# Performance work log

Hardware: AMD Instinct MI355X
Metric: run time of the kernel (lower is better)

The kernel has to match this reference:

```python
import jax, jax.numpy as jnp
from jax import lax
import numpy as np

EPS = 1e-12  # matches torch F.normalize eps


def _dtw_similarity(s1, s2):
    # s1: [L1, D], s2: [L2, D]
    L1, L2 = s1.shape[0], s2.shape[0]
    s1n = s1 / jnp.maximum(jnp.linalg.norm(s1, axis=1, keepdims=True), EPS)
    s2n = s2 / jnp.maximum(jnp.linalg.norm(s2, axis=1, keepdims=True), EPS)
    dist = 1.0 - s1n @ s2n.T  # [L1, L2] cosine distance

    # DTW DP. Row 0 is a cumsum; each subsequent row has a left-to-right
    # sequential dependency handled by an inner scan.
    row0 = jnp.cumsum(dist[0])

    def row_step(prev_row, d_row):
        # prev_row: dtw[i-1, :], d_row: dist[i, :]
        first = prev_row[0] + d_row[0]  # dtw[i, 0]
        # min(prev[j], prev[j-1]) for j >= 1 (vectorized part of the min)
        p = jnp.minimum(prev_row[1:], prev_row[:-1])

        def col_step(c, inp):
            dj, pj = inp
            new = dj + jnp.minimum(pj, c)  # c = dtw[i, j-1]
            return new, new

        _, rest = lax.scan(col_step, first, (d_row[1:], p))
        new_row = jnp.concatenate([first[None], rest])
        return new_row, None

    last_row, _ = lax.scan(row_step, row0, dist[1:])
    dtw_distance = last_row[-1]
    normalized = dtw_distance / (L1 + L2)
    return 1.0 / (1.0 + normalized)


def setup_inputs() -> dict:
    key = jax.random.key(0)
    k1, k2 = jax.random.split(key)
    seq1 = jax.random.normal(k1, (16, 1024, 768), dtype=jnp.float32)
    seq2 = jax.random.normal(k2, (16, 1024, 768), dtype=jnp.float32)
    return {"seq1": seq1, "seq2": seq2}


def reference(seq1, seq2):
    # seq1: [B, L1, D], seq2: [B, L2, D] -> [B]
    return jax.vmap(_dtw_similarity)(seq1, seq2)
```

## Files before the change

### kernel.cpp

```cpp
#include <hip/hip_runtime.h>
#include <hip/hip_bf16.h>

typedef __attribute__((ext_vector_type(4))) float f32x4;
typedef __attribute__((ext_vector_type(8))) short bf16x8;

#define DINF 1e30f

__device__ __forceinline__ unsigned short f2bf(float f) {
    unsigned int u = __builtin_bit_cast(unsigned int, f);
    u += 0x7FFFu + ((u >> 16) & 1u);
    return (unsigned short)(u >> 16);
}

__global__ __launch_bounds__(256) void zero_holes_kernel(float4* __restrict__ skew) {
    const int idx = blockIdx.x;
    const int bt  = idx / 127;
    const int pr  = idx % 127;
    const int h   = pr * 2 + (threadIdx.x >> 7);
    const int row = h < 126 ? h : 1024 + (h - 126);
    const int c   = threadIdx.x & 127;
    skew[((size_t)bt * 1152 + row) * 128 + c] = (float4){0.f, 0.f, 0.f, 0.f};
}

__global__ __launch_bounds__(256) void norm_bf16_kernel(
    const float* __restrict__ s1, const float* __restrict__ s2,
    __hip_bfloat16* __restrict__ o1, __hip_bfloat16* __restrict__ o2) {
    const int gb = blockIdx.x;
    const float* in;
    __hip_bfloat16* out;
    int rowbase;
    if (gb < 4096) { in = s1; out = o1; rowbase = gb * 4; }
    else           { in = s2; out = o2; rowbase = (gb - 4096) * 4; }
    const int wv = threadIdx.x >> 6;
    const int l  = threadIdx.x & 63;
    const int row = rowbase + wv;

    const float* rp = in + (size_t)row * 768 + l * 4;
    float4 x0 = *(const float4*)(rp);
    float4 x1 = *(const float4*)(rp + 256);
    float4 x2 = *(const float4*)(rp + 512);

    float s = x0.x*x0.x + x0.y*x0.y + x0.z*x0.z + x0.w*x0.w
            + x1.x*x1.x + x1.y*x1.y + x1.z*x1.z + x1.w*x1.w
            + x2.x*x2.x + x2.y*x2.y + x2.z*x2.z + x2.w*x2.w;
#pragma unroll
    for (int off = 32; off > 0; off >>= 1) s += __shfl_xor(s, off, 64);

    const float inv = 1.0f / fmaxf(sqrtf(s), 1e-12f);

    __hip_bfloat16* op = out + (size_t)row * 768 + l * 4;
    ushort4 o;
    o.x = f2bf(x0.x*inv); o.y = f2bf(x0.y*inv); o.z = f2bf(x0.z*inv); o.w = f2bf(x0.w*inv);
    *(ushort4*)(op) = o;
    o.x = f2bf(x1.x*inv); o.y = f2bf(x1.y*inv); o.z = f2bf(x1.z*inv); o.w = f2bf(x1.w*inv);
    *(ushort4*)(op + 256) = o;
    o.x = f2bf(x2.x*inv); o.y = f2bf(x2.y*inv); o.z = f2bf(x2.z*inv); o.w = f2bf(x2.w*inv);
    *(ushort4*)(op + 512) = o;
}

#define GLOAD_LDS16(g, l)                                                      \
    __builtin_amdgcn_global_load_lds(                                          \
        (const __attribute__((address_space(1))) void*)(g),                    \
        (__attribute__((address_space(3))) void*)(l), 16, 0, 0)

__global__ __launch_bounds__(256) void gemm_dist_kernel(
    const __hip_bfloat16* __restrict__ A, const __hip_bfloat16* __restrict__ B,
    __hip_bfloat16* __restrict__ skew) {
    __shared__ __hip_bfloat16 lA[128 * 64];
    __shared__ __hip_bfloat16 lB[128 * 64];

    const int blk  = (blockIdx.x & 7) * 128 + (blockIdx.x >> 3);
    const int b    = blk >> 6;
    const int tile = blk & 63;
    const int tm = tile >> 3, tn = tile & 7;
    const int tid  = threadIdx.x;
    const int lane = tid & 63, w = tid >> 6;
    const int lr = lane & 15, lg = lane >> 4;
    const int wm = w >> 1, wn = w & 1;

    const __hip_bfloat16* Ab = A + (size_t)b * (1024 * 768) + (size_t)(tm * 128) * 768;
    const __hip_bfloat16* Bb = B + (size_t)b * (1024 * 768) + (size_t)(tn * 128) * 768;

    const int srow = tid >> 3;
    const int scol = (tid & 7) * 8;

    char* lAb = (char*)lA;
    char* lBb = (char*)lB;

    f32x4 acc[4][4];
#pragma unroll
    for (int m = 0; m < 4; ++m)
#pragma unroll
        for (int n = 0; n < 4; ++n) acc[m][n] = (f32x4){0.f, 0.f, 0.f, 0.f};

    for (int k0 = 0; k0 < 768; k0 += 64) {
#pragma unroll
        for (int q = 0; q < 4; ++q) {
            GLOAD_LDS16(Ab + (size_t)(q * 32 + srow) * 768 + k0 + scol,
                        lAb + q * 4096 + w * 1024);
            GLOAD_LDS16(Bb + (size_t)(q * 32 + srow) * 768 + k0 + scol,
                        lBb + q * 4096 + w * 1024);
        }
        __syncthreads();

#pragma unroll
        for (int ks = 0; ks < 64; ks += 32) {
            bf16x8 af[4], bfr[4];
#pragma unroll
            for (int m = 0; m < 4; ++m)
                af[m] = *(const bf16x8*)&lA[(wm * 64 + m * 16 + lr) * 64 + ks + lg * 8];
#pragma unroll
            for (int n = 0; n < 4; ++n)
                bfr[n] = *(const bf16x8*)&lB[(wn * 64 + n * 16 + lr) * 64 + ks + lg * 8];
#pragma unroll
            for (int m = 0; m < 4; ++m)
#pragma unroll
                for (int n = 0; n < 4; ++n)
                    acc[m][n] = __builtin_amdgcn_mfma_f32_16x16x32_bf16(af[m], bfr[n], acc[m][n], 0, 0, 0);
        }
        __syncthreads();
    }

    unsigned short* S = (unsigned short*)skew + (size_t)b * (1152 * 1024);
#pragma unroll
    for (int m = 0; m < 4; ++m)
#pragma unroll
        for (int n = 0; n < 4; ++n) {
            const int cb = tn * 128 + wn * 64 + n * 16;
            const int soff = 2 * (cb >> 4);
#pragma unroll
            for (int r = 0; r < 4; ++r) {
                const int row = tm * 128 + wm * 64 + m * 16 + lg * 4 + r;
                S[(size_t)(row + soff) * 1024 + cb + lr] = f2bf(1.0f - acc[m][n][r]);
            }
        }
}


#define VWAIT(n) asm volatile("s_waitcnt vmcnt(" #n ")" ::: "memory")

#define GLDMA16(g, l)                                                          \
    __builtin_amdgcn_global_load_lds(                                          \
        (const __attribute__((address_space(1))) void*)(g),                    \
        (__attribute__((address_space(3))) void*)(l), 16, 0, 0)

#define LOADR(BK, SL, RW) do {                                                 \
    const char* g_ = Sb + ((size_t)(RW) << 11);                                \
    GLDMA16(g_,      &ring[BK][SL][0][0]);                                     \
    GLDMA16(g_ + 16, &ring[BK][SL][1][0]);                                     \
} while (0)

#define ISSUE8(BK, BASE) do {                                                  \
    LOADR(BK, 0, (BASE));     LOADR(BK, 1, (BASE) + 1);                        \
    LOADR(BK, 2, (BASE) + 2); LOADR(BK, 3, (BASE) + 3);                        \
    LOADR(BK, 4, (BASE) + 4); LOADR(BK, 5, (BASE) + 5);                        \
    LOADR(BK, 6, (BASE) + 6); LOADR(BK, 7, (BASE) + 7);                        \
} while (0)

#define DSRD(BK, SL, N) do {                                                   \
    N##_0 = ring[BK][SL][0][t]; N##_1 = ring[BK][SL][1][t];                    \
} while (0)

#define STEPBODY(P, E0EXPR) do {                                               \
    unsigned u0_ = __builtin_bit_cast(unsigned, P##_0.x);                      \
    unsigned u1_ = __builtin_bit_cast(unsigned, P##_0.y);                      \
    unsigned u2_ = __builtin_bit_cast(unsigned, P##_0.z);                      \
    unsigned u3_ = __builtin_bit_cast(unsigned, P##_0.w);                      \
    unsigned u4_ = __builtin_bit_cast(unsigned, P##_1.x);                      \
    unsigned u5_ = __builtin_bit_cast(unsigned, P##_1.y);                      \
    unsigned u6_ = __builtin_bit_cast(unsigned, P##_1.z);                      \
    unsigned u7_ = __builtin_bit_cast(unsigned, P##_1.w);                      \
    float d0_  = __builtin_bit_cast(float, u0_ << 16);                         \
    float d1_  = __builtin_bit_cast(float, u0_ & 0xffff0000u);                 \
    float d2_  = __builtin_bit_cast(float, u1_ << 16);                         \
    float d3_  = __builtin_bit_cast(float, u1_ & 0xffff0000u);                 \
    float d4_  = __builtin_bit_cast(float, u2_ << 16);                         \
    float d5_  = __builtin_bit_cast(float, u2_ & 0xffff0000u);                 \
    float d6_  = __builtin_bit_cast(float, u3_ << 16);                         \
    float d7_  = __builtin_bit_cast(float, u3_ & 0xffff0000u);                 \
    float d8_  = __builtin_bit_cast(float, u4_ << 16);                         \
    float d9_  = __builtin_bit_cast(float, u4_ & 0xffff0000u);                 \
    float d10_ = __builtin_bit_cast(float, u5_ << 16);                         \
    float d11_ = __builtin_bit_cast(float, u5_ & 0xffff0000u);                 \
    float d12_ = __builtin_bit_cast(float, u6_ << 16);                         \
    float d13_ = __builtin_bit_cast(float, u6_ & 0xffff0000u);                 \
    float d14_ = __builtin_bit_cast(float, u7_ << 16);                         \
    float d15_ = __builtin_bit_cast(float, u7_ & 0xffff0000u);                 \
    float e0_ = (E0EXPR);                                                      \
    float c0_  = d0_  + e0_;                                                   \
    float c1_  = d1_  + fminf(fminf(p1,  p0),  c0_);                           \
    float c2_  = d2_  + fminf(fminf(p2,  p1),  c1_);                           \
    float c3_  = d3_  + fminf(fminf(p3,  p2),  c2_);                           \
    float c4_  = d4_  + fminf(fminf(p4,  p3),  c3_);                           \
    float c5_  = d5_  + fminf(fminf(p5,  p4),  c4_);                           \
    float c6_  = d6_  + fminf(fminf(p6,  p5),  c5_);                           \
    float c7_  = d7_  + fminf(fminf(p7,  p6),  c6_);                           \
    float c8_  = d8_  + fminf(fminf(p8,  p7),  c7_);                           \
    float c9_  = d9_  + fminf(fminf(p9,  p8),  c8_);                           \
    float c10_ = d10_ + fminf(fminf(p10, p9),  c9_);                           \
    float c11_ = d11_ + fminf(fminf(p11, p10), c10_);                          \
    float c12_ = d12_ + fminf(fminf(p12, p11), c11_);                          \
    float c13_ = d13_ + fminf(fminf(p13, p12), c12_);                          \
    float c14_ = d14_ + fminf(fminf(p14, p13), c13_);                          \
    float c15_ = d15_ + fminf(fminf(p15, p14), c14_);                          \
    p0=c0_; p1=c1_; p2=c2_; p3=c3_; p4=c4_; p5=c5_; p6=c6_; p7=c7_;            \
    p8=c8_; p9=c9_; p10=c10_; p11=c11_; p12=c12_; p13=c13_; p14=c14_; p15=c15_;\
    a3 = a2; a2 = a1;                                                          \
    a1 = __shfl_up(c15_, 1, 64);                                               \
    a1 = lane0 ? DINF : a1;                                                    \
} while (0)

#define STEPB(P)       STEPBODY(P, fminf(fminf(p0, a3), a2))
#define STEPB_FIRST(P) STEPBODY(P, lane0 ? 0.0f : fminf(fminf(p0, a3), a2))

__global__ __launch_bounds__(64, 1) void dtw_dp_kernel(
    const __hip_bfloat16* __restrict__ skew, float* __restrict__ out) {
    __shared__ float4 ring[3][8][2][64];

    const int b = blockIdx.x;
    const int t = threadIdx.x;
    const bool lane0 = (t == 0);
    const char* Sb = (const char*)(skew + (size_t)b * (1152 * 1024)) + (t << 5);

    float p0 = DINF, p1 = DINF, p2 = DINF, p3 = DINF,
          p4 = DINF, p5 = DINF, p6 = DINF, p7 = DINF,
          p8 = DINF, p9 = DINF, p10 = DINF, p11 = DINF,
          p12 = DINF, p13 = DINF, p14 = DINF, p15 = DINF;
    float a1 = DINF, a2 = DINF, a3 = DINF;

    float4 X_0, X_1;
    float4 Y_0, Y_1;

    ISSUE8(0, 0);
    ISSUE8(1, 8);
    VWAIT(16);
    DSRD(0, 0, X); DSRD(0, 1, Y);

    ISSUE8(2, 16);
    STEPB_FIRST(X); DSRD(0, 2, X);
    STEPB(Y);       DSRD(0, 3, Y);
    STEPB(X);       DSRD(0, 4, X);
    STEPB(Y);       DSRD(0, 5, Y);
    STEPB(X);       DSRD(0, 6, X);
    STEPB(Y);       DSRD(0, 7, Y);
    VWAIT(16);
    STEPB(X);       DSRD(1, 0, X);
    STEPB(Y);       DSRD(1, 1, Y);

    int rb = 1, nb = 2, ib = 0, base = 24;
#pragma unroll 1
    for (int j = 1; j < 142; ++j) {
        ISSUE8(ib, base);
        STEPB(X); DSRD(rb, 2, X);
        STEPB(Y); DSRD(rb, 3, Y);
        STEPB(X); DSRD(rb, 4, X);
        STEPB(Y); DSRD(rb, 5, Y);
        STEPB(X); DSRD(rb, 6, X);
        STEPB(Y); DSRD(rb, 7, Y);
        VWAIT(16);
        STEPB(X); DSRD(nb, 0, X);
        STEPB(Y); DSRD(nb, 1, Y);
        const int orb = rb;
        rb = nb; nb = ib; ib = orb;
        base += 8;
    }

    STEPB(X); DSRD(1, 2, X);
    STEPB(Y); DSRD(1, 3, Y);
    STEPB(X); DSRD(1, 4, X);
    STEPB(Y); DSRD(1, 5, Y);
    STEPB(X); DSRD(1, 6, X);
    STEPB(Y); DSRD(1, 7, Y);
    VWAIT(0);
    STEPB(X); DSRD(2, 0, X);
    STEPB(Y); DSRD(2, 1, Y);

    STEPB(X); DSRD(2, 2, X);
    STEPB(Y); DSRD(2, 3, Y);
    STEPB(X); DSRD(2, 4, X);
    STEPB(Y); DSRD(2, 5, Y);
    STEPB(X);
    STEPB(Y);

    if (t == 63) out[b] = 1.0f / (1.0f + p15 * (1.0f / 2048.0f));
}

extern "C" void kernel_launch(void* const* d_in, const int* in_sizes, int n_in,
                              void* d_out, int out_size, void* d_ws, size_t ws_size,
                              hipStream_t stream) {
    const float* s1 = (const float*)d_in[0];
    const float* s2 = (const float*)d_in[1];
    float* out = (float*)d_out;

    char* ws = (char*)d_ws;
    __hip_bfloat16* Abf  = (__hip_bfloat16*)(ws);
    __hip_bfloat16* Bbf  = (__hip_bfloat16*)(ws + 25165824);
    __hip_bfloat16* skew = (__hip_bfloat16*)(ws + 50331648);

    zero_holes_kernel<<<16 * 127, 256, 0, stream>>>((float4*)skew);
    norm_bf16_kernel<<<8192, 256, 0, stream>>>(s1, s2, Abf, Bbf);
    gemm_dist_kernel<<<16 * 64, 256, 0, stream>>>(Abf, Bbf, skew);
    dtw_dp_kernel<<<16, 64, 0, stream>>>(skew, out);
}
```

Baseline: 248.2 us.

## Split DTW wavefront across two waves with LDS boundary exchange

The DP kernel now uses two 64-lane waves per batch. Each lane owns 8 columns instead of 16, and the two waves pass boundary values through a shared-memory ring guarded by barriers. The skewed distance layout is widened to 1296 rows so the second wave's staggered start fits, and the hole-zeroing kernel is replaced by a full hipMemsetAsync of the larger buffer. This halves the serial per-step dependency chain per lane, at the cost of a barrier every 8 steps, more wavefront steps, and a larger memset.

```diff
diff --git a/kernel.cpp b/kernel.cpp
--- a/kernel.cpp
+++ b/kernel.cpp
@@ -10,16 +10,6 @@
     unsigned int u = __builtin_bit_cast(unsigned int, f);
     u += 0x7FFFu + ((u >> 16) & 1u);
     return (unsigned short)(u >> 16);
-}
-
-__global__ __launch_bounds__(256) void zero_holes_kernel(float4* __restrict__ skew) {
-    const int idx = blockIdx.x;
-    const int bt  = idx / 127;
-    const int pr  = idx % 127;
-    const int h   = pr * 2 + (threadIdx.x >> 7);
-    const int row = h < 126 ? h : 1024 + (h - 126);
-    const int c   = threadIdx.x & 127;
-    skew[((size_t)bt * 1152 + row) * 128 + c] = (float4){0.f, 0.f, 0.f, 0.f};
 }
 
 __global__ __launch_bounds__(256) void norm_bf16_kernel(
@@ -121,13 +111,14 @@
         __syncthreads();
     }
 
-    unsigned short* S = (unsigned short*)skew + (size_t)b * (1152 * 1024);
+    unsigned short* S = (unsigned short*)skew + (size_t)b * (1296 * 1024);
 #pragma unroll
     for (int m = 0; m < 4; ++m)
 #pragma unroll
         for (int n = 0; n < 4; ++n) {
             const int cb = tn * 128 + wn * 64 + n * 16;
-            const int soff = 2 * (cb >> 4);
+            const int sbase = ((cb >> 3) << 1) + ((cb >> 9) << 4);
+            const int soff  = sbase + ((lr >> 3) << 1);
 #pragma unroll
             for (int r = 0; r < 4; ++r) {
                 const int row = tm * 128 + wm * 64 + m * 16 + lg * 4 + r;
@@ -138,17 +129,14 @@
 
 
 #define VWAIT(n) asm volatile("s_waitcnt vmcnt(" #n ")" ::: "memory")
+#define SBAR()   asm volatile("s_waitcnt lgkmcnt(0)\n\ts_barrier" ::: "memory")
 
 #define GLDMA16(g, l)                                                          \
     __builtin_amdgcn_global_load_lds(                                          \
         (const __attribute__((address_space(1))) void*)(g),                    \
         (__attribute__((address_space(3))) void*)(l), 16, 0, 0)
 
-#define LOADR(BK, SL, RW) do {                                                 \
-    const char* g_ = Sb + ((size_t)(RW) << 11);                                \
-    GLDMA16(g_,      &ring[BK][SL][0][0]);                                     \
-    GLDMA16(g_ + 16, &ring[BK][SL][1][0]);                                     \
-} while (0)
+#define LOADR(BK, SL, RW) GLDMA16(Sb + ((size_t)(RW) << 11), &ring[w][BK][SL][0])
 
 #define ISSUE8(BK, BASE) do {                                                  \
     LOADR(BK, 0, (BASE));     LOADR(BK, 1, (BASE) + 1);                        \
@@ -157,83 +145,78 @@
     LOADR(BK, 6, (BASE) + 6); LOADR(BK, 7, (BASE) + 7);                        \
 } while (0)
 
-#define DSRD(BK, SL, N) do {                                                   \
-    N##_0 = ring[BK][SL][0][t]; N##_1 = ring[BK][SL][1][t];                    \
+#define DSRD(BK, SL, N) do { N = ring[w][BK][SL][t]; } while (0)
+
+#define STEPCORE(P, E0EXPR) do {                                               \
+    float bf_ = bndp[ro];                         \
+    unsigned u0_ = __builtin_bit_cast(unsigned, P.x);                          \
+    unsigned u1_ = __builtin_bit_cast(unsigned, P.y);                          \
+    unsigned u2_ = __builtin_bit_cast(unsigned, P.z);                          \
+    unsigned u3_ = __builtin_bit_cast(unsigned, P.w);                          \
+    float d0_ = __builtin_bit_cast(float, u0_ << 16);                          \
+    float d1_ = __builtin_bit_cast(float, u0_ & 0xffff0000u);                  \
+    float d2_ = __builtin_bit_cast(float, u1_ << 16);                          \
+    float d3_ = __builtin_bit_cast(float, u1_ & 0xffff0000u);                  \
+    float d4_ = __builtin_bit_cast(float, u2_ << 16);                          \
+    float d5_ = __builtin_bit_cast(float, u2_ & 0xffff0000u);                  \
+    float d6_ = __builtin_bit_cast(float, u3_ << 16);                          \
+    float d7_ = __builtin_bit_cast(float, u3_ & 0xffff0000u);                  \
+    float e0_ = (E0EXPR);                                                      \
+    float c0_ = d0_ + e0_;                                                     \
+    float c1_ = d1_ + fminf(fminf(p1, p0), c0_);                               \
+    float c2_ = d2_ + fminf(fminf(p2, p1), c1_);                               \
+    float c3_ = d3_ + fminf(fminf(p3, p2), c2_);                               \
+    float c4_ = d4_ + fminf(fminf(p4, p3), c3_);                               \
+    float c5_ = d5_ + fminf(fminf(p5, p4), c4_);                               \
+    float c6_ = d6_ + fminf(fminf(p6, p5), c5_);                               \
+    float c7_ = d7_ + fminf(fminf(p7, p6), c6_);                               \
+    bndp[wo] = c7_;                 \
+    p0=c0_; p1=c1_; p2=c2_; p3=c3_; p4=c4_; p5=c5_; p6=c6_; p7=c7_;            \
+    a3 = a2; a2 = a1;                                                          \
+    a1 = __shfl_up(c7_, 1, 64);                                                \
+    float bv_ = isw1 ? b2 : DINF;                      \
+    a1 = lane0 ? bv_ : a1;                                                     \
+    b2 = b1; b1 = bf_;                                                         \
+    ro = (ro + 64) & 2047;                                                     \
+    wo = wbase | ((wo + 64) & 2047);                                           \
 } while (0)
 
-#define STEPBODY(P, E0EXPR) do {                                               \
-    unsigned u0_ = __builtin_bit_cast(unsigned, P##_0.x);                      \
-    unsigned u1_ = __builtin_bit_cast(unsigned, P##_0.y);                      \
-    unsigned u2_ = __builtin_bit_cast(unsigned, P##_0.z);                      \
-    unsigned u3_ = __builtin_bit_cast(unsigned, P##_0.w);                      \
-    unsigned u4_ = __builtin_bit_cast(unsigned, P##_1.x);                      \
-    unsigned u5_ = __builtin_bit_cast(unsigned, P##_1.y);                      \
-    unsigned u6_ = __builtin_bit_cast(unsigned, P##_1.z);                      \
-    unsigned u7_ = __builtin_bit_cast(unsigned, P##_1.w);                      \
-    float d0_  = __builtin_bit_cast(float, u0_ << 16);                         \
-    float d1_  = __builtin_bit_cast(float, u0_ & 0xffff0000u);                 \
-    float d2_  = __builtin_bit_cast(float, u1_ << 16);                         \
-    float d3_  = __builtin_bit_cast(float, u1_ & 0xffff0000u);                 \
-    float d4_  = __builtin_bit_cast(float, u2_ << 16);                         \
-    float d5_  = __builtin_bit_cast(float, u2_ & 0xffff0000u);                 \
-    float d6_  = __builtin_bit_cast(float, u3_ << 16);                         \
-    float d7_  = __builtin_bit_cast(float, u3_ & 0xffff0000u);                 \
-    float d8_  = __builtin_bit_cast(float, u4_ << 16);                         \
-    float d9_  = __builtin_bit_cast(float, u4_ & 0xffff0000u);                 \
-    float d10_ = __builtin_bit_cast(float, u5_ << 16);                         \
-    float d11_ = __builtin_bit_cast(float, u5_ & 0xffff0000u);                 \
-    float d12_ = __builtin_bit_cast(float, u6_ << 16);                         \
-    float d13_ = __builtin_bit_cast(float, u6_ & 0xffff0000u);                 \
-    float d14_ = __builtin_bit_cast(float, u7_ << 16);                         \
-    float d15_ = __builtin_bit_cast(float, u7_ & 0xffff0000u);                 \
-    float e0_ = (E0EXPR);                                                      \
-    float c0_  = d0_  + e0_;                                                   \
-    float c1_  = d1_  + fminf(fminf(p1,  p0),  c0_);                           \
-    float c2_  = d2_  + fminf(fminf(p2,  p1),  c1_);                           \
-    float c3_  = d3_  + fminf(fminf(p3,  p2),  c2_);                           \
-    float c4_  = d4_  + fminf(fminf(p4,  p3),  c3_);                           \
-    float c5_  = d5_  + fminf(fminf(p5,  p4),  c4_);                           \
-    float c6_  = d6_  + fminf(fminf(p6,  p5),  c5_);                           \
-    float c7_  = d7_  + fminf(fminf(p7,  p6),  c6_);                           \
-    float c8_  = d8_  + fminf(fminf(p8,  p7),  c7_);                           \
-    float c9_  = d9_  + fminf(fminf(p9,  p8),  c8_);                           \
-    float c10_ = d10_ + fminf(fminf(p10, p9),  c9_);                           \
-    float c11_ = d11_ + fminf(fminf(p11, p10), c10_);                          \
-    float c12_ = d12_ + fminf(fminf(p12, p11), c11_);                          \
-    float c13_ = d13_ + fminf(fminf(p13, p12), c12_);                          \
-    float c14_ = d14_ + fminf(fminf(p14, p13), c13_);                          \
-    float c15_ = d15_ + fminf(fminf(p15, p14), c14_);                          \
-    p0=c0_; p1=c1_; p2=c2_; p3=c3_; p4=c4_; p5=c5_; p6=c6_; p7=c7_;            \
-    p8=c8_; p9=c9_; p10=c10_; p11=c11_; p12=c12_; p13=c13_; p14=c14_; p15=c15_;\
-    a3 = a2; a2 = a1;                                                          \
-    a1 = __shfl_up(c15_, 1, 64);                                               \
-    a1 = lane0 ? DINF : a1;                                                    \
-} while (0)
-
-#define STEPB(P)       STEPBODY(P, fminf(fminf(p0, a3), a2))
-#define STEPB_FIRST(P) STEPBODY(P, lane0 ? 0.0f : fminf(fminf(p0, a3), a2))
-
-__global__ __launch_bounds__(64, 1) void dtw_dp_kernel(
+#define STEPB(P)       STEPCORE(P, fminf(fminf(p0, a3), a2))
+#define STEPB_FIRST(P) STEPCORE(P, first0 ? 0.0f : fminf(fminf(p0, a3), a2))
+
+__global__ __launch_bounds__(128, 1) void dtw_dp_kernel(
     const __hip_bfloat16* __restrict__ skew, float* __restrict__ out) {
-    __shared__ float4 ring[3][8][2][64];
-
-    const int b = blockIdx.x;
-    const int t = threadIdx.x;
-    const bool lane0 = (t == 0);
-    const char* Sb = (const char*)(skew + (size_t)b * (1152 * 1024)) + (t << 5);
+    __shared__ float4 ring[2][3][8][64];
+    __shared__ float  bnd[2][32][64];
+
+    const int b   = blockIdx.x;
+    const int tid = threadIdx.x;
+    const int w   = tid >> 6;
+    const int t   = tid & 63;
+    const bool lane0  = (t == 0);
+    const bool isw1   = (w == 1);
+    const bool first0 = (tid == 0);
+    const int wbase = w << 11;
+    float* bndp = &bnd[0][0][0];
+
+    const char* Sb = (const char*)skew + (size_t)b * 2654208 + (w << 10) + (t << 4);
+
+#pragma unroll
+    for (int i = 0; i < 32; ++i) bndp[tid + 128 * i] = DINF;
+    SBAR();
 
     float p0 = DINF, p1 = DINF, p2 = DINF, p3 = DINF,
-          p4 = DINF, p5 = DINF, p6 = DINF, p7 = DINF,
-          p8 = DINF, p9 = DINF, p10 = DINF, p11 = DINF,
-          p12 = DINF, p13 = DINF, p14 = DINF, p15 = DINF;
+          p4 = DINF, p5 = DINF, p6 = DINF, p7 = DINF;
     float a1 = DINF, a2 = DINF, a3 = DINF;
-
-    float4 X_0, X_1;
-    float4 Y_0, Y_1;
+    float b1 = DINF, b2 = DINF;
+    int ro = 18 * 64 + 63;
+    int wo = wbase | t;
+
+    float4 X, Y;
 
     ISSUE8(0, 0);
     ISSUE8(1, 8);
-    VWAIT(16);
+    VWAIT(8);
     DSRD(0, 0, X); DSRD(0, 1, Y);
 
     ISSUE8(2, 16);
@@ -243,13 +226,14 @@
     STEPB(Y);       DSRD(0, 5, Y);
     STEPB(X);       DSRD(0, 6, X);
     STEPB(Y);       DSRD(0, 7, Y);
-    VWAIT(16);
+    VWAIT(8);
     STEPB(X);       DSRD(1, 0, X);
     STEPB(Y);       DSRD(1, 1, Y);
 
     int rb = 1, nb = 2, ib = 0, base = 24;
 #pragma unroll 1
-    for (int j = 1; j < 142; ++j) {
+    for (int j = 1; j < 160; ++j) {
+        SBAR();
         ISSUE8(ib, base);
         STEPB(X); DSRD(rb, 2, X);
         STEPB(Y); DSRD(rb, 3, Y);
@@ -257,7 +241,7 @@
         STEPB(Y); DSRD(rb, 5, Y);
         STEPB(X); DSRD(rb, 6, X);
         STEPB(Y); DSRD(rb, 7, Y);
-        VWAIT(16);
+        VWAIT(8);
         STEPB(X); DSRD(nb, 0, X);
         STEPB(Y); DSRD(nb, 1, Y);
         const int orb = rb;
@@ -265,24 +249,26 @@
         base += 8;
     }
 
-    STEPB(X); DSRD(1, 2, X);
-    STEPB(Y); DSRD(1, 3, Y);
-    STEPB(X); DSRD(1, 4, X);
-    STEPB(Y); DSRD(1, 5, Y);
-    STEPB(X); DSRD(1, 6, X);
-    STEPB(Y); DSRD(1, 7, Y);
+    SBAR();
+    STEPB(X); DSRD(rb, 2, X);
+    STEPB(Y); DSRD(rb, 3, Y);
+    STEPB(X); DSRD(rb, 4, X);
+    STEPB(Y); DSRD(rb, 5, Y);
+    STEPB(X); DSRD(rb, 6, X);
+    STEPB(Y); DSRD(rb, 7, Y);
     VWAIT(0);
-    STEPB(X); DSRD(2, 0, X);
-    STEPB(Y); DSRD(2, 1, Y);
-
-    STEPB(X); DSRD(2, 2, X);
-    STEPB(Y); DSRD(2, 3, Y);
-    STEPB(X); DSRD(2, 4, X);
-    STEPB(Y); DSRD(2, 5, Y);
+    STEPB(X); DSRD(nb, 0, X);
+    STEPB(Y); DSRD(nb, 1, Y);
+
+    SBAR();
+    STEPB(X); DSRD(nb, 2, X);
+    STEPB(Y); DSRD(nb, 3, Y);
+    STEPB(X); DSRD(nb, 4, X);
+    STEPB(Y); DSRD(nb, 5, Y);
     STEPB(X);
     STEPB(Y);
 
-    if (t == 63) out[b] = 1.0f / (1.0f + p15 * (1.0f / 2048.0f));
+    if (tid == 127) out[b] = 1.0f / (1.0f + p7 * (1.0f / 2048.0f));
 }
 
 extern "C" void kernel_launch(void* const* d_in, const int* in_sizes, int n_in,
@@ -297,8 +283,9 @@
     __hip_bfloat16* Bbf  = (__hip_bfloat16*)(ws + 25165824);
     __hip_bfloat16* skew = (__hip_bfloat16*)(ws + 50331648);
 
-    zero_holes_kernel<<<16 * 127, 256, 0, stream>>>((float4*)skew);
+    hipMemsetAsync(skew, 0, (size_t)16 * 1296 * 1024 * 2, stream);
+
     norm_bf16_kernel<<<8192, 256, 0, stream>>>(s1, s2, Abf, Bbf);
     gemm_dist_kernel<<<16 * 64, 256, 0, stream>>>(Abf, Bbf, skew);
-    dtw_dp_kernel<<<16, 64, 0, stream>>>(skew, out);
-}
+    dtw_dp_kernel<<<16, 128, 0, stream>>>(skew, out);
+}
```

Result: slower. 285.1 us (+14.9%).
